# Kernel tuning notes

Measured on AMD Instinct MI355X. Metric: run time of the kernel, lower is better.

## Reference

```python
import jax, jax.numpy as jnp
import numpy as np

B, N, FEAT, HID, K, GH, GW = 4, 4096, 64, 128, 16, 256, 256


def setup_inputs() -> dict:
    key = jax.random.key(0)
    ks = jax.random.split(key, 16)
    # N distinct grid cells per batch -> unique sparse coordinates (scn active sites)
    cells = jax.vmap(lambda k: jax.random.permutation(k, GH * GW)[:N])(jax.random.split(ks[0], B))
    cy = (cells // GW).astype(jnp.float32)
    cx = (cells % GW).astype(jnp.float32)
    x = cx / GW  # round(x*GW) == cx exactly
    y = cy / GH
    z = jnp.zeros((B, N), jnp.float32)
    p = jax.random.uniform(ks[1], (B, N), jnp.float32)
    xyzp = jnp.stack([x, y, z, p], axis=-1).astype(jnp.float32)
    features = jax.random.normal(ks[2], (B, N, FEAT), jnp.float32)

    def w(k, shape, s=0.05):
        return (jax.random.normal(k, shape) * s).astype(jnp.float32)

    return {
        "xyzp": xyzp, "features": features,
        "ln_g": jnp.ones((FEAT + 2,), jnp.float32), "ln_b": jnp.zeros((FEAT + 2,), jnp.float32),
        "W1": w(ks[3], (9, FEAT + 2, HID)), "b1": jnp.zeros((HID,), jnp.float32),
        "W2": w(ks[4], (9, HID, 3 * HID)),
        "pe_w1": w(ks[5], (3, HID)), "pe_b1": jnp.zeros((HID,), jnp.float32),
        "pe_w2": w(ks[6], (HID, HID)), "pe_b2": jnp.zeros((HID,), jnp.float32),
        "at_w1": w(ks[7], (HID, HID)), "at_b1": jnp.zeros((HID,), jnp.float32),
        "at_w2": w(ks[8], (HID, HID)), "at_b2": jnp.zeros((HID,), jnp.float32),
        "ag_w": w(ks[9], (HID, FEAT)), "ag_b": jnp.zeros((FEAT,), jnp.float32),
        "mlp_w1": w(ks[10], (FEAT, HID)), "mlp_b1": jnp.zeros((HID,), jnp.float32),
        "mlp_w2": w(ks[11], (HID, FEAT)), "mlp_b2": jnp.zeros((FEAT,), jnp.float32),
    }


def _knn_gather(xf, idx):
    # xf: [B,N,C], idx: [B,N,K] -> [B,N,K,C]
    return xf[jnp.arange(xf.shape[0])[:, None, None], idx]


def _forward(xyzp, features, ln_g, ln_b, W1, b1, W2, pe_w1, pe_b1, pe_w2, pe_b2,
             at_w1, at_b1, at_w2, at_b2, ag_w, ag_b, mlp_w1, mlp_b1, mlp_w2, mlp_b2):
    # knn in (x,y,0) space -> 2D squared distances, K nearest (self included, sorted)
    xy = xyzp[..., :2]
    s = jnp.sum(xy * xy, axis=-1)
    d2 = s[:, :, None] + s[:, None, :] - 2.0 * jnp.einsum('bnd,bmd->bnm', xy, xy)
    idx = jax.lax.top_k(-d2, K)[1]  # [B,N,K]

    # positional encoding of (x,y,p) relative offsets
    xyp = jnp.stack([xyzp[..., 0], xyzp[..., 1], xyzp[..., 3]], axis=-1)  # [B,N,3]
    rel = xyp[:, :, None, :] - _knn_gather(xyp, idx)  # [B,N,K,3]
    pe = jax.nn.relu(rel @ pe_w1 + pe_b1) @ pe_w2 + pe_b2  # [B,N,K,HID]

    # polarity split + LayerNorm
    p = (xyzp[..., 3:4] - 0.5) / 0.5
    sp = jnp.concatenate([jnp.clip(p, 0.0, 1.0), -jnp.clip(p, -1.0, 0.0), features], axis=-1)
    mu = jnp.mean(sp, axis=-1, keepdims=True)
    var = jnp.var(sp, axis=-1, keepdims=True)
    sp = (sp - mu) / jnp.sqrt(var + 1e-5) * ln_g + ln_b  # [B,N,FEAT+2]

    # submanifold 3x3 conv x2 via dense index grid (active sites only)
    cy = jnp.round(xyzp[..., 1] * GH).astype(jnp.int32)
    cx = jnp.round(xyzp[..., 0] * GW).astype(jnp.int32)
    bb = jnp.broadcast_to(jnp.arange(B)[:, None], (B, N))
    grid = jnp.full((B, GH + 2, GW + 2), -1, jnp.int32)
    grid = grid.at[bb, cy + 1, cx + 1].set(jnp.broadcast_to(jnp.arange(N, dtype=jnp.int32)[None], (B, N)))
    off = jnp.arange(-1, 2)
    dy = jnp.repeat(off, 3)  # [9]
    dx = jnp.tile(off, 3)    # [9]
    bi = jnp.arange(B)[:, None, None]
    nbr = grid[bi, cy[:, :, None] + 1 + dy, cx[:, :, None] + 1 + dx]  # [B,N,9]
    mask = nbr >= 0
    safe = jnp.where(mask, nbr, 0)
    m = mask[..., None].astype(sp.dtype)

    g1 = sp[bi, safe] * m                                   # [B,N,9,FEAT+2]
    h1 = jnp.einsum('bnkc,kcd->bnd', g1, W1) + b1           # [B,N,HID]
    g2 = h1[bi, safe] * m                                   # [B,N,9,HID]
    h2 = jnp.einsum('bnkc,kcd->bnd', g2, W2)                # [B,N,3*HID]

    qkv = h2.reshape(B, N, HID, 3)  # matches torch reshape([B,N,-1,3])
    q = qkv[..., 0]
    kk = _knn_gather(qkv[..., 1], idx)
    v = _knn_gather(qkv[..., 2], idx)

    # subtraction-based vector attention scored by MLP, softmax over neighbors
    a = q[:, :, None] - kk + pe
    a = jax.nn.relu(a @ at_w1 + at_b1) @ at_w2 + at_b2
    a = jax.nn.softmax(a / jnp.sqrt(jnp.float32(HID)), axis=-2)

    res = jnp.einsum('bmnf,bmnf->bmf', a, v + pe)
    res = res @ ag_w + ag_b + features
    res = jax.nn.gelu(res @ mlp_w1 + mlp_b1, approximate=False) @ mlp_w2 + mlp_b2 + features
    return res


def reference(xyzp, features, ln_g, ln_b, W1, b1, W2, pe_w1, pe_b1, pe_w2, pe_b2,
              at_w1, at_b1, at_w2, at_b2, ag_w, ag_b, mlp_w1, mlp_b1, mlp_w2, mlp_b2):
    return _forward(xyzp, features, ln_g, ln_b, W1, b1, W2, pe_w1, pe_b1, pe_w2, pe_b2,
                    at_w1, at_b1, at_w2, at_b2, ag_w, ag_b, mlp_w1, mlp_b1, mlp_w2, mlp_b2)
```

## Files before the change

kernel.cpp:

```cpp
#include <hip/hip_runtime.h>
#include <math.h>

#define BB 4
#define NN 4096
#define FEAT 64
#define HID 128
#define KNN 16
#define GS 258
#define CIN 66

typedef __attribute__((ext_vector_type(8))) short bf16x8;
typedef __attribute__((ext_vector_type(4))) float f32x4;
#define MFMA_B16(a, b, c) __builtin_amdgcn_mfma_f32_16x16x32_bf16(a, b, c, 0, 0, 0)

__device__ __forceinline__ short f2b(float f) {
    unsigned u = __builtin_bit_cast(unsigned, f);
    u = (u + 0x7FFFu + ((u >> 16) & 1u)) >> 16;
    return (short)u;
}
__device__ __forceinline__ float b2f(short s) {
    return __builtin_bit_cast(float, ((unsigned)(unsigned short)s) << 16);
}
__device__ __forceinline__ void gload_lds16(const void* g, void* lds) {
    __builtin_amdgcn_global_load_lds((const __attribute__((address_space(1))) unsigned int*)g,
                                     (__attribute__((address_space(3))) unsigned int*)lds, 16, 0, 0);
}

__global__ void k_scatter(const float* __restrict__ xyzp, int* __restrict__ grid, int* __restrict__ cxy) {
    int i = blockIdx.x * 256 + threadIdx.x;
    if (i >= BB * NN) return;
    int b = i / NN;
    float x = xyzp[(size_t)i * 4 + 0], y = xyzp[(size_t)i * 4 + 1];
    int cx = __float2int_rn(x * 256.0f);
    int cy = __float2int_rn(y * 256.0f);
    cxy[i] = cx | (cy << 8);
    grid[b * GS * GS + (cy + 1) * GS + (cx + 1)] = i % NN;
}

__device__ __forceinline__ void ins16(unsigned* a, unsigned key) {
    if (key < a[15]) {
#pragma unroll
        for (int j = 15; j >= 1; --j) {
            unsigned prev = a[j - 1];
            a[j] = (prev > key) ? prev : ((a[j] > key) ? key : a[j]);
        }
        a[0] = a[0] < key ? a[0] : key;
    }
}

__device__ __forceinline__ void cmpex(unsigned& x, unsigned& y) {
    unsigned lo = x < y ? x : y;
    unsigned hi = x < y ? y : x;
    x = lo; y = hi;
}

__device__ __forceinline__ void merge16(const unsigned* L, unsigned* c) {
#pragma unroll
    for (int i = 0; i < 16; ++i) c[i] = L[i];
#pragma unroll
    for (int s = 0; s < 4; ++s) {
        int m = 1 << s;
        unsigned bv[16];
#pragma unroll
        for (int i = 0; i < 16; ++i) bv[i] = __shfl_xor(c[15 - i], m);
#pragma unroll
        for (int i = 0; i < 16; ++i) c[i] = c[i] < bv[i] ? c[i] : bv[i];
#pragma unroll
        for (int d = 8; d >= 1; d >>= 1)
#pragma unroll
            for (int i = 0; i < 16; ++i)
                if (!(i & d)) cmpex(c[i], c[i | d]);
    }
}

__global__ __launch_bounds__(256) void k_knn(const int* __restrict__ grid, const int* __restrict__ cxy,
                                             const float* __restrict__ xyzp, float4* __restrict__ relg) {
    int tid = threadIdx.x;
    int t = tid & 15;
    int q = blockIdx.x * 16 + (tid >> 4);
    int b = q >> 12;
    int me = cxy[q];
    int mx = me & 255, my = (me >> 8) & 255;
    const int* gb = grid + b * GS * GS;
    unsigned L[16];
#pragma unroll
    for (int j = 0; j < 16; j++) L[j] = 0xFFFFFFFFu;
    for (int i = t; i < 441; i += 16) {
        int dy = i / 21 - 10, dx = i % 21 - 10;
        int Y = my + dy, X = mx + dx;
        if ((unsigned)Y >= 256u || (unsigned)X >= 256u) continue;
        int j = gb[(Y + 1) * GS + X + 1];
        if (j >= 0) ins16(L, ((unsigned)(dx * dx + dy * dy) << 12) | (unsigned)j);
    }
    unsigned c[16];
    merge16(L, c);
    for (int r = 11; r <= 256; ++r) {
        bool need = (c[15] >> 12) >= (unsigned)(r * r);
        if (!__any(need)) break;
        if (need) {
            int rr = r * r;
            for (int dx = -r + t; dx <= r; dx += 16) {
                int X = mx + dx;
                if ((unsigned)X >= 256u) continue;
                int d2t = dx * dx + rr;
                int Y0 = my - r, Y1 = my + r;
                if ((unsigned)Y0 < 256u) {
                    int j = gb[(Y0 + 1) * GS + X + 1];
                    if (j >= 0) ins16(L, ((unsigned)d2t << 12) | (unsigned)j);
                }
                if ((unsigned)Y1 < 256u) {
                    int j = gb[(Y1 + 1) * GS + X + 1];
                    if (j >= 0) ins16(L, ((unsigned)d2t << 12) | (unsigned)j);
                }
            }
            for (int dy = -r + 1 + t; dy <= r - 1; dy += 16) {
                int Y = my + dy;
                if ((unsigned)Y >= 256u) continue;
                int rowoff = (Y + 1) * GS;
                int d2s = rr + dy * dy;
                int X0 = mx - r, X1 = mx + r;
                if ((unsigned)X0 < 256u) {
                    int j = gb[rowoff + X0 + 1];
                    if (j >= 0) ins16(L, ((unsigned)d2s << 12) | (unsigned)j);
                }
                if ((unsigned)X1 < 256u) {
                    int j = gb[rowoff + X1 + 1];
                    if (j >= 0) ins16(L, ((unsigned)d2s << 12) | (unsigned)j);
                }
            }
            merge16(L, c);
        }
    }
    unsigned mine = 0;
#pragma unroll
    for (int j = 0; j < 16; ++j)
        if (t == j) mine = c[j];
    int g = (b << 12) | (int)(mine & 4095u);
    float4 mef = *(const float4*)(xyzp + (size_t)q * 4);
    float4 tt = *(const float4*)(xyzp + (size_t)g * 4);
    float4 o;
    o.x = mef.x - tt.x; o.y = mef.y - tt.y; o.z = mef.w - tt.w;
    o.w = __int_as_float(g);
    relg[(size_t)q * 16 + t] = o;
}

#define PK128_SZ (4 * 8 * 512)
#define PKW1_SZ (9 * 3 * 8 * 512)
#define PKW2_SZ (9 * 4 * 24 * 512)

__global__ __launch_bounds__(256) void k_pack(const float* __restrict__ pe_w2, const float* __restrict__ at_w1,
                                              const float* __restrict__ at_w2, const float* __restrict__ W1,
                                              const float* __restrict__ W2,
                                              short* __restrict__ pk_pe2, short* __restrict__ pk_a1,
                                              short* __restrict__ pk_a2, short* __restrict__ pk_w1,
                                              short* __restrict__ pk_w2) {
    int i = blockIdx.x * 256 + threadIdx.x;
    if (i < 3 * PK128_SZ) {
        int seg = i / PK128_SZ, r = i % PK128_SZ;
        int f = r / 512, q = r % 512;
        int lane = q / 8, j = q % 8;
        int kt = f / 8, nt = f % 8;
        int k = kt * 32 + (lane >> 4) * 8 + j, n = nt * 16 + (lane & 15);
        const float* W = (seg == 0) ? pe_w2 : (seg == 1) ? at_w1 : at_w2;
        short* dst = (seg == 0) ? pk_pe2 : (seg == 1) ? pk_a1 : pk_a2;
        dst[r] = f2b(W[k * 128 + n]);
        return;
    }
    i -= 3 * PK128_SZ;
    if (i < PKW1_SZ) {
        int f = i / 512, q = i % 512;
        int lane = q / 8, j = q % 8;
        int tap = f / 24, rem = f % 24;
        int kt = rem / 8, nt = rem % 8;
        int k = kt * 32 + (lane >> 4) * 8 + j, n = nt * 16 + (lane & 15);
        pk_w1[i] = (k < CIN) ? f2b(W1[(tap * CIN + k) * 128 + n]) : (short)0;
        return;
    }
    i -= PKW1_SZ;
    if (i < PKW2_SZ) {
        int f = i / 512, q = i % 512;
        int lane = q / 8, j = q % 8;
        int tap = f / 96, rem = f % 96;
        int kt = rem / 24, nt = rem % 24;
        int k = kt * 32 + (lane >> 4) * 8 + j, n = nt * 16 + (lane & 15);
        pk_w2[i] = f2b(W2[((size_t)(tap * 128 + k)) * 384 + n]);
    }
}

__global__ __launch_bounds__(256) void k_fold(const float* __restrict__ pe_w2, const float* __restrict__ at_w1,
                                              const float* __restrict__ pe_b2, const float* __restrict__ at_b1,
                                              short* __restrict__ pk_wf, float* __restrict__ cf) {
    int bid = blockIdx.x;
    if (bid == 64) {
        int j = threadIdx.x;
        if (j < 128) {
            float acc = at_b1[j];
            for (int m = 0; m < 128; ++m) acc += pe_b2[m] * at_w1[m * 128 + j];
            cf[j] = acc;
        }
        return;
    }
    int idx = bid * 256 + threadIdx.x;
    int i = idx >> 7, j = idx & 127;
    float acc = 0.f;
    for (int m = 0; m < 128; ++m) acc += pe_w2[i * 128 + m] * at_w1[m * 128 + j];
    int lane = (((i >> 3) & 3) << 4) | (j & 15);
    int dst = ((i >> 5) * 8 + (j >> 4)) * 512 + lane * 8 + (i & 7);
    pk_wf[dst] = f2b(acc);
}

__global__ __launch_bounds__(256) void k_sp(const float* __restrict__ xyzp, const float* __restrict__ feat,
                                            const float* __restrict__ ln_g, const float* __restrict__ ln_b,
                                            short* __restrict__ sp_bf) {
    int i = blockIdx.x * 256 + threadIdx.x;
    if (i >= BB * NN) return;
    float v[CIN];
    float p = xyzp[(size_t)i * 4 + 3];
    float pn = (p - 0.5f) * 2.0f;
    v[0] = fminf(fmaxf(pn, 0.0f), 1.0f);
    v[1] = -fminf(fmaxf(pn, -1.0f), 0.0f);
    const float4* f4 = (const float4*)(feat + (size_t)i * FEAT);
#pragma unroll
    for (int j = 0; j < FEAT / 4; j++) {
        float4 t = f4[j];
        v[2 + 4 * j] = t.x; v[3 + 4 * j] = t.y; v[4 + 4 * j] = t.z; v[5 + 4 * j] = t.w;
    }
    float s = 0.0f;
#pragma unroll
    for (int j = 0; j < CIN; j++) s += v[j];
    float mu = s / (float)CIN;
    float vs = 0.0f;
#pragma unroll
    for (int j = 0; j < CIN; j++) { float d = v[j] - mu; vs += d * d; }
    float inv = 1.0f / sqrtf(vs / (float)CIN + 1e-5f);
    unsigned o2[64];
#pragma unroll
    for (int j = 0; j < 33; j++) {
        float a = (v[2 * j] - mu) * inv * ln_g[2 * j] + ln_b[2 * j];
        float bqq = (2 * j + 1 < CIN) ? ((v[2 * j + 1] - mu) * inv * ln_g[2 * j + 1] + ln_b[2 * j + 1]) : 0.f;
        o2[j] = (unsigned)(unsigned short)f2b(a) | (((unsigned)(unsigned short)f2b(bqq)) << 16);
    }
#pragma unroll
    for (int j = 33; j < 64; j++) o2[j] = 0;
    int4* o = (int4*)(sp_bf + (size_t)i * 128);
#pragma unroll
    for (int t = 0; t < 16; t++) o[t] = make_int4(o2[4 * t], o2[4 * t + 1], o2[4 * t + 2], o2[4 * t + 3]);
}

__global__ __launch_bounds__(256) void k_conv1(const int* __restrict__ grid, const int* __restrict__ cxy,
                                               const short* __restrict__ sp_bf, const float* __restrict__ b1,
                                               const short* __restrict__ pk_w1, const short* __restrict__ zero256,
                                               short* __restrict__ h1_bf) {
    __shared__ int sj[9][64];
    __shared__ __align__(16) char sb[2][64 * 256];
    int row0 = blockIdx.x * 64;
    int b = row0 / NN;
    int tid = threadIdx.x;
    int w = tid >> 6, l = tid & 63, cl = l & 15;
    for (int e = tid; e < 9 * 64; e += 256) {
        int k = e / 64, p = e % 64;
        int me = cxy[row0 + p];
        sj[k][p] = grid[b * GS * GS + (((me >> 8) & 255) + k / 3) * GS + ((me & 255) + k % 3)];
    }
    __syncthreads();
    f32x4 acc[4][2];
#pragma unroll
    for (int m = 0; m < 4; m++)
#pragma unroll
        for (int nt = 0; nt < 2; nt++) acc[m][nt] = (f32x4){0.f, 0.f, 0.f, 0.f};

#define STAGE1(bufp, tap)                                                                      \
    {                                                                                          \
        _Pragma("unroll") for (int i = 0; i < 4; ++i) {                                        \
            int row = w * 16 + i * 4 + (l >> 4);                                               \
            int j = sj[tap][row];                                                              \
            int srcch = cl ^ (row & 7);                                                        \
            const short* src = (j >= 0) ? (sp_bf + ((size_t)(b * NN + j) * 128 + srcch * 8))   \
                                        : (zero256 + srcch * 8);                               \
            gload_lds16(src, (bufp) + (w * 16 + i * 4) * 256);                                 \
        }                                                                                      \
    }
    STAGE1(&sb[0][0], 0);
    asm volatile("s_waitcnt vmcnt(0)" ::: "memory");
    __syncthreads();
    int cur = 0;
    for (int tap = 0; tap < 9; ++tap) {
        if (tap < 8) STAGE1(&sb[cur ^ 1][0], tap + 1);
        const char* base = &sb[cur][0];
#pragma unroll
        for (int kt = 0; kt < 3; ++kt) {
            bf16x8 a[4];
#pragma unroll
            for (int m = 0; m < 4; ++m) {
                int row = m * 16 + (l & 15);
                a[m] = *(const bf16x8*)&base[row * 256 + ((kt * 64 + (l >> 4) * 16) ^ ((row & 7) << 4))];
            }
#pragma unroll
            for (int nt = 0; nt < 2; ++nt) {
                bf16x8 bv = *(const bf16x8*)(pk_w1 + (size_t)(((tap * 3 + kt) * 8 + w * 2 + nt) * 64 + l) * 8);
#pragma unroll
                for (int m = 0; m < 4; ++m) acc[m][nt] = MFMA_B16(a[m], bv, acc[m][nt]);
            }
        }
        asm volatile("s_waitcnt vmcnt(0)" ::: "memory");
        __syncthreads();
        cur ^= 1;
    }
#pragma unroll
    for (int nt = 0; nt < 2; ++nt) {
        int col = (w * 2 + nt) * 16 + cl;
        float bb = b1[col];
#pragma unroll
        for (int m = 0; m < 4; ++m)
#pragma unroll
            for (int j = 0; j < 4; ++j) {
                int row = row0 + m * 16 + (l >> 4) * 4 + j;
                h1_bf[(size_t)row * 128 + col] = f2b(acc[m][nt][j] + bb);
            }
    }
}

__global__ __launch_bounds__(256) void k_conv2(const int* __restrict__ grid, const int* __restrict__ cxy,
                                               const short* __restrict__ h1_bf, const short* __restrict__ pk_w2,
                                               const short* __restrict__ zero256,
                                               short* __restrict__ qg, short* __restrict__ kg, short* __restrict__ vg) {
    __shared__ int sj[9][64];
    __shared__ __align__(16) char sb[2][64 * 256];
    int bid = blockIdx.x;
    int nb = bid % 3, mb = bid / 3;
    int row0 = mb * 64;
    int b = row0 / NN;
    int tid = threadIdx.x;
    int w = tid >> 6, l = tid & 63, cl = l & 15;
    for (int e = tid; e < 9 * 64; e += 256) {
        int k = e / 64, p = e % 64;
        int me = cxy[row0 + p];
        sj[k][p] = grid[b * GS * GS + (((me >> 8) & 255) + k / 3) * GS + ((me & 255) + k % 3)];
    }
    __syncthreads();
    f32x4 acc[4][2];
#pragma unroll
    for (int m = 0; m < 4; m++)
#pragma unroll
        for (int nt = 0; nt < 2; nt++) acc[m][nt] = (f32x4){0.f, 0.f, 0.f, 0.f};

#define STAGE2(bufp, tap)                                                                      \
    {                                                                                          \
        _Pragma("unroll") for (int i = 0; i < 4; ++i) {                                        \
            int row = w * 16 + i * 4 + (l >> 4);                                               \
            int j = sj[tap][row];                                                              \
            int srcch = cl ^ (row & 7);                                                        \
            const short* src = (j >= 0) ? (h1_bf + ((size_t)(b * NN + j) * 128 + srcch * 8))   \
                                        : (zero256 + srcch * 8);                               \
            gload_lds16(src, (bufp) + (w * 16 + i * 4) * 256);                                 \
        }                                                                                      \
    }
    STAGE2(&sb[0][0], 0);
    asm volatile("s_waitcnt vmcnt(0)" ::: "memory");
    __syncthreads();
    int cur = 0;
    for (int tap = 0; tap < 9; ++tap) {
        if (tap < 8) STAGE2(&sb[cur ^ 1][0], tap + 1);
        const char* base = &sb[cur][0];
#pragma unroll
        for (int kt = 0; kt < 4; ++kt) {
            bf16x8 a[4];
#pragma unroll
            for (int m = 0; m < 4; ++m) {
                int row = m * 16 + (l & 15);
                a[m] = *(const bf16x8*)&base[row * 256 + ((kt * 64 + (l >> 4) * 16) ^ ((row & 7) << 4))];
            }
#pragma unroll
            for (int nt = 0; nt < 2; ++nt) {
                bf16x8 bv = *(const bf16x8*)(pk_w2 + (size_t)(((tap * 4 + kt) * 24 + nb * 8 + w * 2 + nt) * 64 + l) * 8);
#pragma unroll
                for (int m = 0; m < 4; ++m) acc[m][nt] = MFMA_B16(a[m], bv, acc[m][nt]);
            }
        }
        asm volatile("s_waitcnt vmcnt(0)" ::: "memory");
        __syncthreads();
        cur ^= 1;
    }
#pragma unroll
    for (int nt = 0; nt < 2; ++nt) {
        int col = nb * 128 + (w * 2 + nt) * 16 + cl;
        int s = col % 3, dd = col / 3;
        short* dst = (s == 0) ? qg : (s == 1) ? kg : vg;
#pragma unroll
        for (int m = 0; m < 4; ++m)
#pragma unroll
            for (int j = 0; j < 4; ++j) {
                int row = row0 + m * 16 + (l >> 4) * 4 + j;
                dst[(size_t)row * 128 + dd] = f2b(acc[m][nt][j]);
            }
    }
}

__global__ __launch_bounds__(256) void k_qk1(const short* __restrict__ qg, const short* __restrict__ kg,
                                             const short* __restrict__ pk_a1, const float* __restrict__ cf,
                                             short* __restrict__ q1, short* __restrict__ k1) {
    __shared__ __align__(16) char sb[64 * 256];
    int bid = blockIdx.x;
    int qmode = (bid < 256);
    int row0 = (bid & 255) * 64;
    const short* S = qmode ? qg : kg;
    short* O = qmode ? q1 : k1;
    int tid = threadIdx.x;
    int w = tid >> 6, l = tid & 63, cl = l & 15;
    for (int e = tid; e < 1024; e += 256) {
        int row = e >> 4, sl = e & 15;
        gload_lds16(S + ((size_t)(row0 + row) * 128 + (sl ^ (row & 7)) * 8), &sb[e * 16]);
    }
    asm volatile("s_waitcnt vmcnt(0)" ::: "memory");
    __syncthreads();
    f32x4 acc[4][2];
#pragma unroll
    for (int m = 0; m < 4; m++)
#pragma unroll
        for (int nt = 0; nt < 2; nt++) acc[m][nt] = (f32x4){0.f, 0.f, 0.f, 0.f};
#pragma unroll
    for (int kt = 0; kt < 4; ++kt) {
        bf16x8 a[4];
#pragma unroll
        for (int m = 0; m < 4; ++m) {
            int row = m * 16 + (l & 15);
            a[m] = *(const bf16x8*)&sb[row * 256 + ((kt * 64 + (l >> 4) * 16) ^ ((row & 7) << 4))];
        }
#pragma unroll
        for (int nt = 0; nt < 2; ++nt) {
            bf16x8 bv = *(const bf16x8*)(pk_a1 + (size_t)((kt * 8 + w * 2 + nt) * 64 + l) * 8);
#pragma unroll
            for (int m = 0; m < 4; ++m) acc[m][nt] = MFMA_B16(a[m], bv, acc[m][nt]);
        }
    }
#pragma unroll
    for (int nt = 0; nt < 2; ++nt) {
        int a = w * 2 + nt;
        int col = a * 16 + cl;
        float cv = qmode ? cf[col] : 0.f;
#pragma unroll
        for (int m = 0; m < 4; ++m)
#pragma unroll
            for (int j = 0; j < 4; ++j) {
                int row = row0 + m * 16 + (l >> 4) * 4 + j;
                int off = qmode ? (cl * 8 + a) : col;
                O[(size_t)row * 128 + off] = f2b(acc[m][nt][j] + cv);
            }
    }
}

__global__ __launch_bounds__(256, 3) void k_attn(const float4* __restrict__ relg,
                                                 const short* __restrict__ q1g, const short* __restrict__ k1g,
                                                 const short* __restrict__ vg,
                                                 const float* __restrict__ pe_w1, const float* __restrict__ pe_b1,
                                                 const float* __restrict__ pe_b2, const float* __restrict__ at_b2,
                                                 const short* __restrict__ pk_pe2, const short* __restrict__ pk_wf,
                                                 const short* __restrict__ pk_a2, float* __restrict__ res1) {
    __shared__ __align__(16) char s_work[4 * 4096];
    __shared__ __align__(16) char s_kv[4 * 4096];
    __shared__ float4 s_rel[64];
    int tid = threadIdx.x;
    int w = tid >> 6, l = tid & 63, cl = l & 15;
    int P = blockIdx.x * 4 + w;
    char* WK = s_work + w * 4096;
    char* KV = s_kv + w * 4096;

    int g_reg = 0;
    if (l < 16) {
        float4 f4 = relg[(size_t)P * 16 + l];
        s_rel[w * 16 + l] = f4;
        g_reg = __float_as_int(f4.w);
    }
#pragma unroll
    for (int it = 0; it < 4; ++it) {
        int row = it * 4 + (l >> 4);
        int g = __shfl(g_reg, row);
        int srcch = cl ^ (row & 7);
        gload_lds16(k1g + (size_t)g * 128 + srcch * 8, KV + it * 1024);
    }
    bf16x8 q1f = *(const bf16x8*)(q1g + (size_t)P * 128 + cl * 8);
    {
        int c0 = 2 * l;
        float wa0 = pe_w1[c0], wa1 = pe_w1[c0 + 1];
        float wb0 = pe_w1[128 + c0], wb1 = pe_w1[129 + c0];
        float wc0 = pe_w1[256 + c0], wc1 = pe_w1[257 + c0];
        float ba0 = pe_b1[c0], ba1 = pe_b1[c0 + 1];
#pragma unroll
        for (int lr = 0; lr < 16; ++lr) {
            float4 rel = s_rel[w * 16 + lr];
            float h0 = fmaxf(rel.x * wa0 + rel.y * wb0 + rel.z * wc0 + ba0, 0.f);
            float h1v = fmaxf(rel.x * wa1 + rel.y * wb1 + rel.z * wc1 + ba1, 0.f);
            unsigned pk = (unsigned)(unsigned short)f2b(h0) | (((unsigned)(unsigned short)f2b(h1v)) << 16);
            *(unsigned*)&WK[lr * 256 + ((4 * l) ^ ((lr & 7) << 4))] = pk;
        }
    }
    int ra = l & 15;
    unsigned pe_pk[8][2];
    {
        f32x4 pacc[8];
#pragma unroll
        for (int nt = 0; nt < 8; nt++) pacc[nt] = (f32x4){0.f, 0.f, 0.f, 0.f};
#pragma unroll
        for (int kt = 0; kt < 4; ++kt) {
            int off = kt * 64 + (l >> 4) * 16;
            bf16x8 a0 = *(const bf16x8*)&WK[ra * 256 + (off ^ ((ra & 7) << 4))];
#pragma unroll
            for (int nt = 0; nt < 8; ++nt) {
                bf16x8 bv = *(const bf16x8*)(pk_pe2 + (size_t)((kt * 8 + nt) * 64 + l) * 8);
                pacc[nt] = MFMA_B16(a0, bv, pacc[nt]);
            }
        }
#pragma unroll
        for (int nt = 0; nt < 8; ++nt) {
            float b2v = pe_b2[nt * 16 + cl];
            float p0v = pacc[nt][0] + b2v, p1v = pacc[nt][1] + b2v;
            float p2v = pacc[nt][2] + b2v, p3v = pacc[nt][3] + b2v;
            pe_pk[nt][0] = (unsigned)(unsigned short)f2b(p0v) | (((unsigned)(unsigned short)f2b(p1v)) << 16);
            pe_pk[nt][1] = (unsigned)(unsigned short)f2b(p2v) | (((unsigned)(unsigned short)f2b(p3v)) << 16);
        }
    }
    f32x4 facc[8];
#pragma unroll
    for (int nt = 0; nt < 8; nt++) facc[nt] = (f32x4){0.f, 0.f, 0.f, 0.f};
#pragma unroll
    for (int kt = 0; kt < 4; ++kt) {
        int off = kt * 64 + (l >> 4) * 16;
        bf16x8 a0 = *(const bf16x8*)&WK[ra * 256 + (off ^ ((ra & 7) << 4))];
#pragma unroll
        for (int nt = 0; nt < 8; ++nt) {
            bf16x8 bv = *(const bf16x8*)(pk_wf + (size_t)((kt * 8 + nt) * 64 + l) * 8);
            facc[nt] = MFMA_B16(a0, bv, facc[nt]);
        }
    }
    asm volatile("s_waitcnt vmcnt(0)" ::: "memory");
#pragma unroll
    for (int nt = 0; nt < 8; ++nt) {
        int col = nt * 16 + cl;
        float qv = b2f(q1f[nt]);
#pragma unroll
        for (int j = 0; j < 4; ++j) {
            int lr = (l >> 4) * 4 + j;
            float kv = b2f(*(const short*)&KV[lr * 256 + ((col * 2) ^ ((lr & 7) << 4))]);
            float x = facc[nt][j] + qv - kv;
            *(short*)&WK[lr * 256 + ((col * 2) ^ ((lr & 7) << 4))] = f2b(fmaxf(x, 0.f));
        }
    }
    asm volatile("s_waitcnt lgkmcnt(0)" ::: "memory");
#pragma unroll
    for (int it = 0; it < 4; ++it) {
        int row = it * 4 + (l >> 4);
        int g = __shfl(g_reg, row);
        int srcch = cl ^ (row & 7);
        gload_lds16(vg + (size_t)g * 128 + srcch * 8, KV + it * 1024);
    }
#pragma unroll
    for (int nt = 0; nt < 8; nt++) facc[nt] = (f32x4){0.f, 0.f, 0.f, 0.f};
#pragma unroll
    for (int kt = 0; kt < 4; ++kt) {
        int off = kt * 64 + (l >> 4) * 16;
        bf16x8 a0 = *(const bf16x8*)&WK[ra * 256 + (off ^ ((ra & 7) << 4))];
#pragma unroll
        for (int nt = 0; nt < 8; ++nt) {
            bf16x8 bv = *(const bf16x8*)(pk_a2 + (size_t)((kt * 8 + nt) * 64 + l) * 8);
            facc[nt] = MFMA_B16(a0, bv, facc[nt]);
        }
    }
    asm volatile("s_waitcnt vmcnt(0)" ::: "memory");
    const float scale = 0.08838834764831845f;
#pragma unroll
    for (int nt = 0; nt < 8; ++nt) {
        int col = nt * 16 + cl;
        float bv = at_b2[col];
        float vv[4];
#pragma unroll
        for (int j = 0; j < 4; ++j) vv[j] = (facc[nt][j] + bv) * scale;
        float m = fmaxf(fmaxf(vv[0], vv[1]), fmaxf(vv[2], vv[3]));
        m = fmaxf(m, __shfl_xor(m, 16));
        m = fmaxf(m, __shfl_xor(m, 32));
        float ee[4], es = 0.f;
#pragma unroll
        for (int j = 0; j < 4; ++j) { ee[j] = __expf(vv[j] - m); es += ee[j]; }
        es += __shfl_xor(es, 16);
        es += __shfl_xor(es, 32);
        float pev[4];
        pev[0] = b2f((short)(pe_pk[nt][0] & 0xffff));
        pev[1] = b2f((short)(pe_pk[nt][0] >> 16));
        pev[2] = b2f((short)(pe_pk[nt][1] & 0xffff));
        pev[3] = b2f((short)(pe_pk[nt][1] >> 16));
        float o = 0.f;
#pragma unroll
        for (int j = 0; j < 4; ++j) {
            int lr = (l >> 4) * 4 + j;
            float vvv = b2f(*(const short*)&KV[lr * 256 + ((col * 2) ^ ((lr & 7) << 4))]);
            o += ee[j] * (vvv + pev[j]);
        }
        o += __shfl_xor(o, 16);
        o += __shfl_xor(o, 32);
        if (l < 16) res1[(size_t)P * 128 + col] = o / es;
    }
}

__global__ __launch_bounds__(256) void k_head(const float* __restrict__ res1, const float* __restrict__ feat,
                                              const float* __restrict__ ag_w, const float* __restrict__ ag_b,
                                              const float* __restrict__ mlp_w1, const float* __restrict__ mlp_b1,
                                              const float* __restrict__ mlp_w2, const float* __restrict__ mlp_b2,
                                              float* __restrict__ out) {
    __shared__ __align__(16) float rs[64][128];
    __shared__ __align__(16) float r1s[64][64];
    int tid = threadIdx.x;
    int i0 = blockIdx.x * 64;
    for (int e = tid; e < 64 * 128; e += 256) rs[e >> 7][e & 127] = res1[(size_t)i0 * 128 + e];
    __syncthreads();
    {
        int d = tid & 63, rg = tid >> 6;
        float acc[16];
#pragma unroll
        for (int i = 0; i < 16; i++) acc[i] = 0.0f;
        for (int c4 = 0; c4 < 32; ++c4) {
            int c = c4 * 4;
            float w0 = ag_w[c * 64 + d], w1 = ag_w[(c + 1) * 64 + d];
            float w2 = ag_w[(c + 2) * 64 + d], w3 = ag_w[(c + 3) * 64 + d];
#pragma unroll
            for (int i = 0; i < 16; i++) {
                float4 f = *(const float4*)&rs[rg * 16 + i][c];
                acc[i] += f.x * w0 + f.y * w1 + f.z * w2 + f.w * w3;
            }
        }
        float bb = ag_b[d];
#pragma unroll
        for (int i = 0; i < 16; i++) {
            int pp = rg * 16 + i;
            r1s[pp][d] = acc[i] + bb + feat[(size_t)(i0 + pp) * 64 + d];
        }
    }
    __syncthreads();
    {
        int d = tid & 127, rg = tid >> 7;
        float acc[32];
#pragma unroll
        for (int i = 0; i < 32; i++) acc[i] = 0.0f;
        for (int c4 = 0; c4 < 16; ++c4) {
            int c = c4 * 4;
            float w0 = mlp_w1[c * 128 + d], w1 = mlp_w1[(c + 1) * 128 + d];
            float w2 = mlp_w1[(c + 2) * 128 + d], w3 = mlp_w1[(c + 3) * 128 + d];
#pragma unroll
            for (int i = 0; i < 32; i++) {
                float4 f = *(const float4*)&r1s[rg * 32 + i][c];
                acc[i] += f.x * w0 + f.y * w1 + f.z * w2 + f.w * w3;
            }
        }
        float bb = mlp_b1[d];
#pragma unroll
        for (int i = 0; i < 32; i++) {
            float x = acc[i] + bb;
            rs[rg * 32 + i][d] = 0.5f * x * (1.0f + erff(x * 0.70710678118654752f));
        }
    }
    __syncthreads();
    {
        int d = tid & 63, rg = tid >> 6;
        float acc[16];
#pragma unroll
        for (int i = 0; i < 16; i++) acc[i] = 0.0f;
        for (int c4 = 0; c4 < 32; ++c4) {
            int c = c4 * 4;
            float w0 = mlp_w2[c * 64 + d], w1 = mlp_w2[(c + 1) * 64 + d];
            float w2 = mlp_w2[(c + 2) * 64 + d], w3 = mlp_w2[(c + 3) * 64 + d];
#pragma unroll
            for (int i = 0; i < 16; i++) {
                float4 f = *(const float4*)&rs[rg * 16 + i][c];
                acc[i] += f.x * w0 + f.y * w1 + f.z * w2 + f.w * w3;
            }
        }
        float bb = mlp_b2[d];
#pragma unroll
        for (int i = 0; i < 16; i++) {
            int pp = rg * 16 + i;
            out[(size_t)(i0 + pp) * 64 + d] = acc[i] + bb + feat[(size_t)(i0 + pp) * 64 + d];
        }
    }
}

extern "C" void kernel_launch(void* const* d_in, const int* in_sizes, int n_in,
                              void* d_out, int out_size, void* d_ws, size_t ws_size,
                              hipStream_t stream) {
    const float* xyzp = (const float*)d_in[0];
    const float* features = (const float*)d_in[1];
    const float* ln_g = (const float*)d_in[2];
    const float* ln_b = (const float*)d_in[3];
    const float* W1 = (const float*)d_in[4];
    const float* b1 = (const float*)d_in[5];
    const float* W2 = (const float*)d_in[6];
    const float* pe_w1 = (const float*)d_in[7];
    const float* pe_b1 = (const float*)d_in[8];
    const float* pe_w2 = (const float*)d_in[9];
    const float* pe_b2 = (const float*)d_in[10];
    const float* at_w1 = (const float*)d_in[11];
    const float* at_b1 = (const float*)d_in[12];
    const float* at_w2 = (const float*)d_in[13];
    const float* at_b2 = (const float*)d_in[14];
    const float* ag_w = (const float*)d_in[15];
    const float* ag_b = (const float*)d_in[16];
    const float* mlp_w1 = (const float*)d_in[17];
    const float* mlp_b1 = (const float*)d_in[18];
    const float* mlp_w2 = (const float*)d_in[19];
    const float* mlp_b2 = (const float*)d_in[20];
    float* out = (float*)d_out;

    char* w = (char*)d_ws;
    auto alloc = [&](size_t bytes) { char* pp = w; w += (bytes + 255) & ~(size_t)255; return pp; };
    int* grid = (int*)alloc((size_t)BB * GS * GS * 4);
    short* zero256 = (short*)alloc(256);
    int* cxy = (int*)alloc((size_t)BB * NN * 4);
    float4* relg = (float4*)alloc((size_t)BB * NN * KNN * 16);
    short* sp_bf = (short*)alloc((size_t)BB * NN * 128 * 2);
    short* h1_bf = (short*)alloc((size_t)BB * NN * HID * 2);
    short* qg = (short*)alloc((size_t)BB * NN * HID * 2);
    short* kg = (short*)alloc((size_t)BB * NN * HID * 2);
    short* vg = (short*)alloc((size_t)BB * NN * HID * 2);
    short* q1 = (short*)alloc((size_t)BB * NN * HID * 2);
    short* k1 = (short*)alloc((size_t)BB * NN * HID * 2);
    float* res1 = (float*)alloc((size_t)BB * NN * HID * 4);
    short* pk_pe2 = (short*)alloc((size_t)PK128_SZ * 2);
    short* pk_a1 = (short*)alloc((size_t)PK128_SZ * 2);
    short* pk_a2 = (short*)alloc((size_t)PK128_SZ * 2);
    short* pk_wf = (short*)alloc((size_t)PK128_SZ * 2);
    short* pk_w1 = (short*)alloc((size_t)PKW1_SZ * 2);
    short* pk_w2 = (short*)alloc((size_t)PKW2_SZ * 2);
    float* cf = (float*)alloc(128 * 4);

    hipMemsetAsync(grid, 0xFF, (size_t)BB * GS * GS * 4, stream);
    hipMemsetAsync(zero256, 0, 256, stream);
    k_scatter<<<(BB * NN + 255) / 256, 256, 0, stream>>>(xyzp, grid, cxy);
    k_pack<<<(3 * PK128_SZ + PKW1_SZ + PKW2_SZ + 255) / 256, 256, 0, stream>>>(
        pe_w2, at_w1, at_w2, W1, W2, pk_pe2, pk_a1, pk_a2, pk_w1, pk_w2);
    k_fold<<<65, 256, 0, stream>>>(pe_w2, at_w1, pe_b2, at_b1, pk_wf, cf);
    k_knn<<<BB * NN / 16, 256, 0, stream>>>(grid, cxy, xyzp, relg);
    k_sp<<<(BB * NN + 255) / 256, 256, 0, stream>>>(xyzp, features, ln_g, ln_b, sp_bf);
    k_conv1<<<BB * NN / 64, 256, 0, stream>>>(grid, cxy, sp_bf, b1, pk_w1, zero256, h1_bf);
    k_conv2<<<(BB * NN / 64) * 3, 256, 0, stream>>>(grid, cxy, h1_bf, pk_w2, zero256, qg, kg, vg);
    k_qk1<<<512, 256, 0, stream>>>(qg, kg, pk_a1, cf, q1, k1);
    k_attn<<<BB * NN / 4, 256, 0, stream>>>(relg, q1, k1, vg, pe_w1, pe_b1, pe_b2, at_b2,
                                            pk_pe2, pk_wf, pk_a2, res1);
    k_head<<<BB * NN / 64, 256, 0, stream>>>(res1, features, ag_w, ag_b, mlp_w1, mlp_b1, mlp_w2, mlp_b2, out);
}
```

Baseline: 244.2 us.

## Gather K and V neighbor rows straight into registers via interleaved channel layout

The q/k/v projection now writes V, and the k_qk1 kernel now writes K1, in a transposed channel layout (cl*8 + a). Each lane can then load one 16-byte vector per neighbor holding exactly the columns it needs in the MFMA output layout. The attention kernel drops the per-wave LDS staging buffer for K and V, along with its async global-to-LDS loads and waits, and issues all K and V gathers up front into registers. This halves LDS use and removes LDS reads, but raises register pressure and moves the wait on the global gathers to their first use.

```diff
diff --git a/kernel.cpp b/kernel.cpp
--- a/kernel.cpp
+++ b/kernel.cpp
@@ -385,13 +385,14 @@
     for (int nt = 0; nt < 2; ++nt) {
         int col = nb * 128 + (w * 2 + nt) * 16 + cl;
         int s = col % 3, dd = col / 3;
-        short* dst = (s == 0) ? qg : (s == 1) ? kg : vg;
 #pragma unroll
         for (int m = 0; m < 4; ++m)
 #pragma unroll
             for (int j = 0; j < 4; ++j) {
                 int row = row0 + m * 16 + (l >> 4) * 4 + j;
-                dst[(size_t)row * 128 + dd] = f2b(acc[m][nt][j]);
+                if (s == 0) qg[(size_t)row * 128 + dd] = f2b(acc[m][nt][j]);
+                else if (s == 1) kg[(size_t)row * 128 + dd] = f2b(acc[m][nt][j]);
+                else vg[(size_t)row * 128 + (dd & 15) * 8 + (dd >> 4)] = f2b(acc[m][nt][j]);
             }
     }
 }
@@ -443,8 +444,7 @@
 #pragma unroll
             for (int j = 0; j < 4; ++j) {
                 int row = row0 + m * 16 + (l >> 4) * 4 + j;
-                int off = qmode ? (cl * 8 + a) : col;
-                O[(size_t)row * 128 + off] = f2b(acc[m][nt][j] + cv);
+                O[(size_t)row * 128 + cl * 8 + a] = f2b(acc[m][nt][j] + cv);
             }
     }
 }
@@ -457,13 +457,11 @@
                                                  const short* __restrict__ pk_pe2, const short* __restrict__ pk_wf,
                                                  const short* __restrict__ pk_a2, float* __restrict__ res1) {
     __shared__ __align__(16) char s_work[4 * 4096];
-    __shared__ __align__(16) char s_kv[4 * 4096];
     __shared__ float4 s_rel[64];
     int tid = threadIdx.x;
     int w = tid >> 6, l = tid & 63, cl = l & 15;
     int P = blockIdx.x * 4 + w;
     char* WK = s_work + w * 4096;
-    char* KV = s_kv + w * 4096;
 
     int g_reg = 0;
     if (l < 16) {
@@ -471,12 +469,12 @@
         s_rel[w * 16 + l] = f4;
         g_reg = __float_as_int(f4.w);
     }
-#pragma unroll
-    for (int it = 0; it < 4; ++it) {
-        int row = it * 4 + (l >> 4);
-        int g = __shfl(g_reg, row);
-        int srcch = cl ^ (row & 7);
-        gload_lds16(k1g + (size_t)g * 128 + srcch * 8, KV + it * 1024);
+    bf16x8 k1f[4], vf[4];
+#pragma unroll
+    for (int j = 0; j < 4; ++j) {
+        int g = __shfl(g_reg, (l >> 4) * 4 + j);
+        k1f[j] = *(const bf16x8*)(k1g + (size_t)g * 128 + cl * 8);
+        vf[j] = *(const bf16x8*)(vg + (size_t)g * 128 + cl * 8);
     }
     bf16x8 q1f = *(const bf16x8*)(q1g + (size_t)P * 128 + cl * 8);
     {
@@ -532,7 +530,6 @@
             facc[nt] = MFMA_B16(a0, bv, facc[nt]);
         }
     }
-    asm volatile("s_waitcnt vmcnt(0)" ::: "memory");
 #pragma unroll
     for (int nt = 0; nt < 8; ++nt) {
         int col = nt * 16 + cl;
@@ -540,18 +537,9 @@
 #pragma unroll
         for (int j = 0; j < 4; ++j) {
             int lr = (l >> 4) * 4 + j;
-            float kv = b2f(*(const short*)&KV[lr * 256 + ((col * 2) ^ ((lr & 7) << 4))]);
-            float x = facc[nt][j] + qv - kv;
+            float x = facc[nt][j] + qv - b2f(k1f[j][nt]);
             *(short*)&WK[lr * 256 + ((col * 2) ^ ((lr & 7) << 4))] = f2b(fmaxf(x, 0.f));
         }
-    }
-    asm volatile("s_waitcnt lgkmcnt(0)" ::: "memory");
-#pragma unroll
-    for (int it = 0; it < 4; ++it) {
-        int row = it * 4 + (l >> 4);
-        int g = __shfl(g_reg, row);
-        int srcch = cl ^ (row & 7);
-        gload_lds16(vg + (size_t)g * 128 + srcch * 8, KV + it * 1024);
     }
 #pragma unroll
     for (int nt = 0; nt < 8; nt++) facc[nt] = (f32x4){0.f, 0.f, 0.f, 0.f};
@@ -565,7 +553,6 @@
             facc[nt] = MFMA_B16(a0, bv, facc[nt]);
         }
     }
-    asm volatile("s_waitcnt vmcnt(0)" ::: "memory");
     const float scale = 0.08838834764831845f;
 #pragma unroll
     for (int nt = 0; nt < 8; ++nt) {
@@ -589,11 +576,7 @@
         pev[3] = b2f((short)(pe_pk[nt][1] >> 16));
         float o = 0.f;
 #pragma unroll
-        for (int j = 0; j < 4; ++j) {
-            int lr = (l >> 4) * 4 + j;
-            float vvv = b2f(*(const short*)&KV[lr * 256 + ((col * 2) ^ ((lr & 7) << 4))]);
-            o += ee[j] * (vvv + pev[j]);
-        }
+        for (int j = 0; j < 4; ++j) o += ee[j] * (b2f(vf[j][nt]) + pev[j]);
         o += __shfl_xor(o, 16);
         o += __shfl_xor(o, 32);
         if (l < 16) res1[(size_t)P * 128 + col] = o / es;
```

After: 241.5 us. Within noise of the previous version (-1.1%).
